# Kernel tuning notes

Hardware: AMD Instinct MI355X
Metric: run time of the kernel (lower is better)

The kernel has to match this reference:

```python
import jax, jax.numpy as jnp
import numpy as np

S, B, H = 2048, 2, 1024
NH = 16
HD = H // NH
EPS = 1e-5


def _ln(z, w, b):
    m = jnp.mean(z, axis=-1, keepdims=True)
    v = jnp.mean(jnp.square(z - m), axis=-1, keepdims=True)
    return (z - m) * jax.lax.rsqrt(v + EPS) * w + b


def setup_inputs() -> dict:
    key = jax.random.key(0)
    ks = jax.random.split(key, 8)
    std = 0.02
    return {
        "x": jax.random.normal(ks[0], (S, B, H), dtype=jnp.float32),
        "ln1_w": jnp.ones((H,), jnp.float32),
        "ln1_b": jnp.zeros((H,), jnp.float32),
        "w_qkv": jax.random.normal(ks[1], (3 * H, H), jnp.float32) * std,
        "b_qkv": jnp.zeros((3 * H,), jnp.float32),
        "w_proj": jax.random.normal(ks[2], (H, H), jnp.float32) * std,
        "b_proj": jnp.zeros((H,), jnp.float32),
        "ln2_w": jnp.ones((H,), jnp.float32),
        "ln2_b": jnp.zeros((H,), jnp.float32),
        "w_fc1": jax.random.normal(ks[3], (4 * H, H), jnp.float32) * std,
        "b_fc1": jnp.zeros((4 * H,), jnp.float32),
        "w_fc2": jax.random.normal(ks[4], (H, 4 * H), jnp.float32) * std,
        "b_fc2": jnp.zeros((H,), jnp.float32),
    }


def reference(x, ln1_w, ln1_b, w_qkv, b_qkv, w_proj, b_proj,
              ln2_w, ln2_b, w_fc1, b_fc1, w_fc2, b_fc2):
    s, b, h = x.shape
    # --- LayerNormLinear: LN then fused QKV projection ---
    residual = x
    qkv = _ln(x, ln1_w, ln1_b) @ w_qkv.T + b_qkv            # [S, B, 3H]
    # per-head interleaved packing: [S, B, NH, 3*HD] then split on last dim
    qkv = qkv.reshape(s, b, NH, 3 * HD).transpose(1, 2, 0, 3)  # [B, NH, S, 3HD]
    q, k, v = jnp.split(qkv, 3, axis=3)                      # each [B, NH, S, HD]
    # --- naive causal attention with full SxS scores ---
    scores = jnp.einsum("bhsd,bhtd->bhst", q, k) * (HD ** -0.5)
    causal = jnp.triu(jnp.ones((s, s), dtype=bool), k=1)
    scores = jnp.where(causal, -jnp.inf, scores)
    attn = jax.nn.softmax(scores, axis=-1)                   # [B, NH, S, S]
    out = jnp.einsum("bhst,bhtd->bhsd", attn, v)             # [B, NH, S, HD]
    out = out.transpose(0, 2, 1, 3).reshape(b, s, h).transpose(1, 0, 2)  # [S, B, H]
    out = out @ w_proj.T + b_proj
    x = residual + out
    # --- LayerNormMLP: LN -> fc1 -> gelu(tanh) -> fc2, residual ---
    residual = x
    hmid = jax.nn.gelu(_ln(x, ln2_w, ln2_b) @ w_fc1.T + b_fc1, approximate=True)
    x = residual + (hmid @ w_fc2.T + b_fc2)
    return x
```

## Files before the change

### kernel.cpp

```cpp
#include <hip/hip_runtime.h>
#include <math.h>

#define S_LEN 2048
#define B_SZ 2
#define NHEAD 16
#define HDIM 64
#define H_DIM 1024
#define M_ROWS (S_LEN * B_SZ)
#define LN_EPS 1e-5f
#define KSTR 72
#define SCL 0.18033688011112042f

typedef __attribute__((ext_vector_type(4))) float f32x4;
typedef __attribute__((ext_vector_type(8))) short short8;
typedef __attribute__((ext_vector_type(8))) unsigned short u16x8;
typedef __attribute__((ext_vector_type(4))) unsigned short u16x4;
typedef __attribute__((ext_vector_type(2))) unsigned short u16x2;

typedef __attribute__((address_space(3))) unsigned int lds_u32;
typedef const __attribute__((address_space(1))) unsigned int glb_u32;

__device__ __forceinline__ float bf2f(unsigned short u) {
    return __uint_as_float(((unsigned int)u) << 16);
}
__device__ __forceinline__ unsigned short f2bf(float f) {
    unsigned int u = __float_as_uint(f);
    return (unsigned short)((u + 0x7fffu + ((u >> 16) & 1u)) >> 16);
}

__global__ __launch_bounds__(256) void cast_all(const float* __restrict__ wqkv,
                                                const float* __restrict__ wproj,
                                                const float* __restrict__ wfc1,
                                                const float* __restrict__ wfc2,
                                                unsigned short* __restrict__ oqkv,
                                                unsigned short* __restrict__ oproj,
                                                unsigned short* __restrict__ ofc1,
                                                unsigned short* __restrict__ ofc2) {
    const int i = blockIdx.x * 256 + threadIdx.x;
    const float* src; unsigned short* dst; int off;
    if (i < 786432)       { src = wqkv;  dst = oqkv;  off = i; }
    else if (i < 1048576) { src = wproj; dst = oproj; off = i - 786432; }
    else if (i < 2097152) { src = wfc1;  dst = ofc1;  off = i - 1048576; }
    else                  { src = wfc2;  dst = ofc2;  off = i - 2097152; }
    f32x4 v = ((const f32x4*)src)[off];
    u16x4 o;
    o.x = f2bf(v.x); o.y = f2bf(v.y); o.z = f2bf(v.z); o.w = f2bf(v.w);
    ((u16x4*)dst)[off] = o;
}

__global__ __launch_bounds__(256) void ln_bf16(const float* __restrict__ x,
                                               const float* __restrict__ w,
                                               const float* __restrict__ b,
                                               unsigned short* __restrict__ y) {
    const int m = blockIdx.x;
    const int tid = threadIdx.x;
    const float* row = x + (size_t)m * H_DIM;

    float4 v = ((const float4*)row)[tid];
    float s  = v.x + v.y + v.z + v.w;
    float ss = v.x * v.x + v.y * v.y + v.z * v.z + v.w * v.w;

    __shared__ float rs[4], rss[4], stats[2];
    const int wave = tid >> 6, lane = tid & 63;
    for (int off = 32; off; off >>= 1) {
        s  += __shfl_down(s, off);
        ss += __shfl_down(ss, off);
    }
    if (lane == 0) { rs[wave] = s; rss[wave] = ss; }
    __syncthreads();
    if (tid == 0) {
        float S = rs[0] + rs[1] + rs[2] + rs[3];
        float SS = rss[0] + rss[1] + rss[2] + rss[3];
        float mean = S * (1.0f / H_DIM);
        float var = SS * (1.0f / H_DIM) - mean * mean;
        stats[0] = mean;
        stats[1] = rsqrtf(var + LN_EPS);
    }
    __syncthreads();
    const float mean = stats[0], inv = stats[1];
    float4 wv = ((const float4*)w)[tid];
    float4 bv = ((const float4*)b)[tid];
    u16x4 o;
    o.x = f2bf((v.x - mean) * inv * wv.x + bv.x);
    o.y = f2bf((v.y - mean) * inv * wv.y + bv.y);
    o.z = f2bf((v.z - mean) * inv * wv.z + bv.z);
    o.w = f2bf((v.w - mean) * inv * wv.w + bv.w);
    ((u16x4*)(y + (size_t)m * H_DIM))[tid] = o;
}

template <int EPI, bool BF_OUT, int TN>
__global__ __launch_bounds__(256) void gemm_mfma(const unsigned short* __restrict__ A,
                                                 const unsigned short* __restrict__ B,
                                                 const float* __restrict__ bias,
                                                 const float* __restrict__ resid,
                                                 void* __restrict__ Cout,
                                                 int M, int N, int K) {
    constexpr int NJ  = TN / 32;
    constexpr int ANI = 4;
    constexpr int BNI = TN / 32;
    __shared__ __attribute__((aligned(16))) unsigned short As0[128 * 64];
    __shared__ __attribute__((aligned(16))) unsigned short Bs0[TN * 64];
    __shared__ __attribute__((aligned(16))) unsigned short As1[128 * 64];
    __shared__ __attribute__((aligned(16))) unsigned short Bs1[TN * 64];

    const int tid = threadIdx.x;
    const int wid = tid >> 6;
    const int ln  = tid & 63;
    const int quad = ln >> 4;
    const int mr   = ln & 15;
    const int wm = (wid >> 1) * 64;
    const int wn = (wid & 1) * (TN / 2);

    const int mb = M >> 7;
    const int stripe = mb >> 3;
    const int xcd = blockIdx.x & 7;
    const int local = blockIdx.x >> 3;
    const int m0 = (xcd * stripe + (local % stripe)) << 7;
    const int n0 = (local / stripe) * TN;

    const int lr = ln >> 3, lc = ln & 7;
    const size_t Kb = (size_t)K * 2;
    const char* gA = (const char*)A + (size_t)(m0 + wid * 32 + lr) * Kb
                     + (size_t)((lc << 4) ^ (lr << 4));
    const int bwr = (TN == 128) ? wid * 32 : wid * 16;
    const char* gB = (const char*)B + (size_t)(n0 + bwr + lr) * Kb
                     + (size_t)((lc << 4) ^ (lr << 4));

    auto stage = [&](int kt, unsigned short* As_, unsigned short* Bs_) {
        const char* pa = gA + (size_t)kt * 128;
        unsigned int* la = (unsigned int*)As_ + wid * (ANI * 256);
#pragma unroll
        for (int i = 0; i < ANI; i++)
            __builtin_amdgcn_global_load_lds((glb_u32*)(pa + (size_t)i * 8 * Kb),
                                             (lds_u32*)(la + i * 256), 16, 0, 0);
        const char* pb = gB + (size_t)kt * 128;
        unsigned int* lb = (unsigned int*)Bs_ + wid * (BNI * 256);
#pragma unroll
        for (int i = 0; i < BNI; i++)
            __builtin_amdgcn_global_load_lds((glb_u32*)(pb + (size_t)i * 8 * Kb),
                                             (lds_u32*)(lb + i * 256), 16, 0, 0);
    };

    const f32x4 zero = {0.f, 0.f, 0.f, 0.f};
    f32x4 acc[4][NJ];
#pragma unroll
    for (int i = 0; i < 4; i++)
#pragma unroll
        for (int j = 0; j < NJ; j++) acc[i][j] = zero;

    const int swz = (mr & 7) << 3;
    auto compute = [&](const unsigned short* As_, const unsigned short* Bs_) {
#pragma unroll
        for (int h = 0; h < 2; h++) {
            short8 af[4], bfr[NJ];
#pragma unroll
            for (int i = 0; i < 4; i++)
                af[i] = *(const short8*)(As_ + (wm + i * 16 + mr) * 64
                                             + ((h * 32 + quad * 8) ^ swz));
#pragma unroll
            for (int j = 0; j < NJ; j++)
                bfr[j] = *(const short8*)(Bs_ + (wn + j * 16 + mr) * 64
                                              + ((h * 32 + quad * 8) ^ swz));
#pragma unroll
            for (int i = 0; i < 4; i++)
#pragma unroll
                for (int j = 0; j < NJ; j++)
                    acc[i][j] = __builtin_amdgcn_mfma_f32_16x16x32_bf16(bfr[j], af[i], acc[i][j], 0, 0, 0);
        }
    };

    const int nt = K >> 6;
    stage(0, As0, Bs0);
    __syncthreads();
    for (int kt = 0; kt < nt; kt += 2) {
        stage(kt + 1, As1, Bs1);
        compute(As0, Bs0);
        __syncthreads();
        if (kt + 2 < nt) stage(kt + 2, As0, Bs0);
        compute(As1, Bs1);
        if (kt + 2 < nt) __syncthreads();
    }

    f32x4 bias4[NJ];
#pragma unroll
    for (int j = 0; j < NJ; j++)
        bias4[j] = *(const f32x4*)(bias + n0 + wn + j * 16 + quad * 4);

#pragma unroll
    for (int i = 0; i < 4; i++) {
        const int m = m0 + wm + i * 16 + mr;
#pragma unroll
        for (int j = 0; j < NJ; j++) {
            const int nb = n0 + wn + j * 16 + quad * 4;
            f32x4 v = acc[i][j] + bias4[j];
            if (EPI == 1) v += *(const f32x4*)(resid + (size_t)m * N + nb);
            if (EPI == 2) {
#pragma unroll
                for (int r = 0; r < 4; r++) {
                    const float t = v[r];
                    const float u = t + 0.044715f * t * t * t;
                    const float e = exp2f(2.3022112f * u);
                    v[r] = t - t / (e + 1.0f);
                }
            }
            if (BF_OUT) {
                u16x4 pk;
                pk.x = f2bf(v.x); pk.y = f2bf(v.y); pk.z = f2bf(v.z); pk.w = f2bf(v.w);
                *(u16x4*)((unsigned short*)Cout + (size_t)m * N + nb) = pk;
            } else {
                *(f32x4*)((float*)Cout + (size_t)m * N + nb) = v;
            }
        }
    }
}

__global__ __launch_bounds__(256) void attn_mfma(const unsigned short* __restrict__ qkv,
                                                 unsigned short* __restrict__ out) {
    __shared__ __attribute__((aligned(16))) unsigned short Ks[64 * KSTR];
    __shared__ __attribute__((aligned(16))) unsigned short Vs[64 * KSTR];
    __shared__ __attribute__((aligned(16))) unsigned short Ps[64 * KSTR];

    const int tid = threadIdx.x;
    const int wid = tid >> 6;
    const int ln  = tid & 63;
    const int quad = ln >> 4;
    const int mr   = ln & 15;

    const int id = blockIdx.x;
    const int local = id >> 3;
    const int bh = (id & 7) * 4 + (local >> 4);
    const int pa = local & 15;
    const int b  = bh >> 4;
    const int nh = bh & 15;
    const size_t chan = (size_t)nh * 192;

    const int ksr = tid >> 2, ksc = tid & 3;
    const int vt0 = (tid & 31) * 2, vd0 = (tid >> 5) * 8;

    u16x8 kp0, kp1, vp0, vp1;

#pragma unroll
    for (int half = 0; half < 2; half++) {
        const int qt = half ? (31 - pa) : pa;
        const int qb = qt * 64;

        short8 qf0, qf1;
        {
            const int qrow = qb + wid * 16 + mr;
            const unsigned short* gq = qkv + ((size_t)(qrow * 2 + b)) * 3072 + chan + quad * 8;
            qf0 = *(const short8*)gq;
            qf1 = *(const short8*)(gq + 32);
        }

        const f32x4 zero = {0.f, 0.f, 0.f, 0.f};
        f32x4 o[4];
        float ps = 0.f;
#pragma unroll
        for (int d = 0; d < 4; d++) o[d] = zero;

        {
            const unsigned short* gk = qkv + ((size_t)(ksr * 2 + b)) * 3072 + chan + 64 + ksc * 16;
            kp0 = *(const u16x8*)gk;
            kp1 = *(const u16x8*)(gk + 8);
            const unsigned short* gv = qkv + ((size_t)(vt0 * 2 + b)) * 3072 + chan + 128 + vd0;
            vp0 = *(const u16x8*)gv;
            vp1 = *(const u16x8*)(gv + 6144);
        }

        for (int kt = 0; kt <= qt; kt++) {
            __syncthreads();
            *(u16x8*)(Ks + ksr * KSTR + ksc * 16) = kp0;
            *(u16x8*)(Ks + ksr * KSTR + ksc * 16 + 8) = kp1;
#pragma unroll
            for (int j = 0; j < 8; j++) {
                u16x2 pr; pr.x = vp0[j]; pr.y = vp1[j];
                *(u16x2*)(Vs + (vd0 + j) * KSTR + vt0) = pr;
            }
            if (kt < qt) {
                const int nb = (kt + 1) * 64;
                const unsigned short* gk =
                    qkv + ((size_t)((nb + ksr) * 2 + b)) * 3072 + chan + 64 + ksc * 16;
                kp0 = *(const u16x8*)gk;
                kp1 = *(const u16x8*)(gk + 8);
                const unsigned short* gv =
                    qkv + ((size_t)((nb + vt0) * 2 + b)) * 3072 + chan + 128 + vd0;
                vp0 = *(const u16x8*)gv;
                vp1 = *(const u16x8*)(gv + 6144);
            }
            __syncthreads();

            f32x4 sacc[4];
#pragma unroll
            for (int n = 0; n < 4; n++) {
                sacc[n] = zero;
                const unsigned short* kb = Ks + (n * 16 + mr) * KSTR + quad * 8;
                short8 kfr0 = *(const short8*)kb;
                short8 kfr1 = *(const short8*)(kb + 32);
                sacc[n] = __builtin_amdgcn_mfma_f32_16x16x32_bf16(kfr0, qf0, sacc[n], 0, 0, 0);
                sacc[n] = __builtin_amdgcn_mfma_f32_16x16x32_bf16(kfr1, qf1, sacc[n], 0, 0, 0);
            }
            if (kt == qt) {
#pragma unroll
                for (int n = 0; n < 4; n++)
#pragma unroll
                    for (int r = 0; r < 4; r++)
                        if (n * 16 + quad * 4 + r > wid * 16 + mr) sacc[n][r] = -3.0e38f;
            }

            unsigned short* prow = Ps + (wid * 16 + mr) * KSTR + quad * 4;
#pragma unroll
            for (int n = 0; n < 4; n++) {
                u16x4 pk;
#pragma unroll
                for (int r = 0; r < 4; r++) {
                    const float p = exp2f(fminf(sacc[n][r] * SCL, 80.f));
                    ps += p;
                    pk[r] = (unsigned short)(__float_as_uint(p) >> 16);
                }
                *(u16x4*)(prow + n * 16) = pk;
            }

            {
                const unsigned short* pb = Ps + (wid * 16 + mr) * KSTR + quad * 8;
                short8 pa0 = *(const short8*)pb;
                short8 pa1 = *(const short8*)(pb + 32);
#pragma unroll
                for (int d = 0; d < 4; d++) {
                    const unsigned short* vb = Vs + (d * 16 + mr) * KSTR + quad * 8;
                    short8 vf0 = *(const short8*)vb;
                    short8 vf1 = *(const short8*)(vb + 32);
                    o[d] = __builtin_amdgcn_mfma_f32_16x16x32_bf16(vf0, pa0, o[d], 0, 0, 0);
                    o[d] = __builtin_amdgcn_mfma_f32_16x16x32_bf16(vf1, pa1, o[d], 0, 0, 0);
                }
            }
        }

        ps += __shfl_xor(ps, 16);
        ps += __shfl_xor(ps, 32);
        const float inv = 1.0f / ps;
        const int qrow = qb + wid * 16 + mr;
        unsigned short* po = out + ((size_t)(qrow * 2 + b)) * H_DIM + nh * HDIM;
#pragma unroll
        for (int d = 0; d < 4; d++) {
            u16x4 pk;
#pragma unroll
            for (int r = 0; r < 4; r++) pk[r] = f2bf(o[d][r] * inv);
            *(u16x4*)(po + d * 16 + quad * 4) = pk;
        }
    }
}

extern "C" void kernel_launch(void* const* d_in, const int* in_sizes, int n_in,
                              void* d_out, int out_size, void* d_ws, size_t ws_size,
                              hipStream_t stream) {
    const float* x      = (const float*)d_in[0];
    const float* ln1_w  = (const float*)d_in[1];
    const float* ln1_b  = (const float*)d_in[2];
    const float* w_qkv  = (const float*)d_in[3];
    const float* b_qkv  = (const float*)d_in[4];
    const float* w_proj = (const float*)d_in[5];
    const float* b_proj = (const float*)d_in[6];
    const float* ln2_w  = (const float*)d_in[7];
    const float* ln2_b  = (const float*)d_in[8];
    const float* w_fc1  = (const float*)d_in[9];
    const float* b_fc1  = (const float*)d_in[10];
    const float* w_fc2  = (const float*)d_in[11];
    const float* b_fc2  = (const float*)d_in[12];
    float* out = (float*)d_out;

    char* ws = (char*)d_ws;
    unsigned short* wqkv_bf  = (unsigned short*)(ws);
    unsigned short* wproj_bf = (unsigned short*)(ws + ((size_t)6 << 20));
    unsigned short* wfc1_bf  = (unsigned short*)(ws + ((size_t)8 << 20));
    unsigned short* wfc2_bf  = (unsigned short*)(ws + ((size_t)16 << 20));
    unsigned short* ln_buf   = (unsigned short*)(ws + ((size_t)24 << 20));
    unsigned short* qkv_bf   = (unsigned short*)(ws + ((size_t)32 << 20));
    unsigned short* attn_bf  = (unsigned short*)(ws + ((size_t)56 << 20));
    unsigned short* fc1_bf   = (unsigned short*)(ws + ((size_t)32 << 20));

    cast_all<<<12288, 256, 0, stream>>>(w_qkv, w_proj, w_fc1, w_fc2,
                                        wqkv_bf, wproj_bf, wfc1_bf, wfc2_bf);

    ln_bf16<<<M_ROWS, 256, 0, stream>>>(x, ln1_w, ln1_b, ln_buf);
    gemm_mfma<0, true, 128><<<768, 256, 0, stream>>>(
        ln_buf, wqkv_bf, b_qkv, nullptr, qkv_bf, M_ROWS, 3072, 1024);
    attn_mfma<<<512, 256, 0, stream>>>(qkv_bf, attn_bf);
    gemm_mfma<1, false, 64><<<512, 256, 0, stream>>>(
        attn_bf, wproj_bf, b_proj, x, out, M_ROWS, 1024, 1024);
    ln_bf16<<<M_ROWS, 256, 0, stream>>>(out, ln2_w, ln2_b, ln_buf);
    gemm_mfma<2, true, 128><<<1024, 256, 0, stream>>>(
        ln_buf, wfc1_bf, b_fc1, nullptr, fc1_bf, M_ROWS, 4096, 1024);
    gemm_mfma<1, false, 64><<<512, 256, 0, stream>>>(
        fc1_bf, wfc2_bf, b_fc2, out, out, M_ROWS, 1024, 4096);
}
```

Before: 344.5 us.

## Use multi-buffered GEMM pipeline with explicit vmcnt waits

Restructures the MFMA GEMM main loop from a double-buffer, two-barrier scheme into a ring of 2 or 3 LDS buffers (3 when TN is 64). Each iteration waits with an explicit s_waitcnt vmcnt count so only the current tile's async global-to-LDS loads must be complete, and later tiles stay in flight. The goal is to hide more global load latency behind compute. In exchange it uses more LDS per block, which can lower occupancy, and its correctness depends on hand-computed vmcnt constants matching the number of issued loads.

```diff
diff --git a/kernel.cpp b/kernel.cpp
--- a/kernel.cpp
+++ b/kernel.cpp
@@ -19,6 +19,8 @@
 
 typedef __attribute__((address_space(3))) unsigned int lds_u32;
 typedef const __attribute__((address_space(1))) unsigned int glb_u32;
+
+#define ASM_VMCNT(N) asm volatile("s_waitcnt vmcnt(" #N ")" ::: "memory")
 
 __device__ __forceinline__ float bf2f(unsigned short u) {
     return __uint_as_float(((unsigned int)u) << 16);
@@ -98,10 +100,9 @@
     constexpr int NJ  = TN / 32;
     constexpr int ANI = 4;
     constexpr int BNI = TN / 32;
-    __shared__ __attribute__((aligned(16))) unsigned short As0[128 * 64];
-    __shared__ __attribute__((aligned(16))) unsigned short Bs0[TN * 64];
-    __shared__ __attribute__((aligned(16))) unsigned short As1[128 * 64];
-    __shared__ __attribute__((aligned(16))) unsigned short Bs1[TN * 64];
+    constexpr int NBUF = (TN == 128) ? 2 : 3;
+    __shared__ __attribute__((aligned(16))) unsigned short As[NBUF][128 * 64];
+    __shared__ __attribute__((aligned(16))) unsigned short Bs[NBUF][TN * 64];
 
     const int tid = threadIdx.x;
     const int wid = tid >> 6;
@@ -126,15 +127,15 @@
     const char* gB = (const char*)B + (size_t)(n0 + bwr + lr) * Kb
                      + (size_t)((lc << 4) ^ (lr << 4));
 
-    auto stage = [&](int kt, unsigned short* As_, unsigned short* Bs_) {
+    auto stage = [&](int kt, int buf) {
         const char* pa = gA + (size_t)kt * 128;
-        unsigned int* la = (unsigned int*)As_ + wid * (ANI * 256);
+        unsigned int* la = (unsigned int*)&As[buf][0] + wid * (ANI * 256);
 #pragma unroll
         for (int i = 0; i < ANI; i++)
             __builtin_amdgcn_global_load_lds((glb_u32*)(pa + (size_t)i * 8 * Kb),
                                              (lds_u32*)(la + i * 256), 16, 0, 0);
         const char* pb = gB + (size_t)kt * 128;
-        unsigned int* lb = (unsigned int*)Bs_ + wid * (BNI * 256);
+        unsigned int* lb = (unsigned int*)&Bs[buf][0] + wid * (BNI * 256);
 #pragma unroll
         for (int i = 0; i < BNI; i++)
             __builtin_amdgcn_global_load_lds((glb_u32*)(pb + (size_t)i * 8 * Kb),
@@ -170,15 +171,27 @@
     };
 
     const int nt = K >> 6;
-    stage(0, As0, Bs0);
-    __syncthreads();
-    for (int kt = 0; kt < nt; kt += 2) {
-        stage(kt + 1, As1, Bs1);
-        compute(As0, Bs0);
-        __syncthreads();
-        if (kt + 2 < nt) stage(kt + 2, As0, Bs0);
-        compute(As1, Bs1);
-        if (kt + 2 < nt) __syncthreads();
+    stage(0, 0);
+    stage(1, 1);
+    if (NBUF == 3) stage(2, 2);
+
+    int cb = 0;
+    for (int kt = 0; kt < nt; kt++) {
+        if (NBUF == 3) {
+            if (kt + 2 < nt)      ASM_VMCNT(12);
+            else if (kt + 1 < nt) ASM_VMCNT(6);
+            else                  ASM_VMCNT(0);
+        } else {
+            if (kt + 1 < nt)      ASM_VMCNT(8);
+            else                  ASM_VMCNT(0);
+        }
+        __builtin_amdgcn_s_barrier();
+        __builtin_amdgcn_sched_barrier(0);
+        compute(&As[cb][0], &Bs[cb][0]);
+        __builtin_amdgcn_sched_barrier(0);
+        __builtin_amdgcn_s_barrier();
+        if (kt + NBUF < nt) stage(kt + NBUF, cb);
+        cb = (cb + 1 == NBUF) ? 0 : cb + 1;
     }
 
     f32x4 bias4[NJ];
```

Result: no change. 339.2 us (-1.5%).

## Load GEMM B operand directly into registers and hand-pipeline A staging with vmcnt waits

Applied to the files above, without the earlier changes.

The GEMM no longer stages B tiles through LDS. Each lane reads its B fragments straight from global memory into registers one k-tile ahead, while A stays double-buffered in LDS via global_load_lds. Explicit s_waitcnt vmcnt counts, raw s_barrier and sched_barrier replace __syncthreads so loads overlap compute, and launch bounds request 3 blocks per CU. This cuts LDS traffic and footprint, but the B global loads are less coalesced, register pressure rises, and the hand-tuned vmcnt counts are fragile to get right.

```diff
diff --git a/kernel.cpp b/kernel.cpp
--- a/kernel.cpp
+++ b/kernel.cpp
@@ -19,6 +19,8 @@
 
 typedef __attribute__((address_space(3))) unsigned int lds_u32;
 typedef const __attribute__((address_space(1))) unsigned int glb_u32;
+
+#define ASM_VMCNT(N) asm volatile("s_waitcnt vmcnt(" #N ")" ::: "memory")
 
 __device__ __forceinline__ float bf2f(unsigned short u) {
     return __uint_as_float(((unsigned int)u) << 16);
@@ -89,19 +91,15 @@
 }
 
 template <int EPI, bool BF_OUT, int TN>
-__global__ __launch_bounds__(256) void gemm_mfma(const unsigned short* __restrict__ A,
-                                                 const unsigned short* __restrict__ B,
-                                                 const float* __restrict__ bias,
-                                                 const float* __restrict__ resid,
-                                                 void* __restrict__ Cout,
-                                                 int M, int N, int K) {
+__global__ __launch_bounds__(256, 3) void gemm_mfma(const unsigned short* __restrict__ A,
+                                                    const unsigned short* __restrict__ B,
+                                                    const float* __restrict__ bias,
+                                                    const float* __restrict__ resid,
+                                                    void* __restrict__ Cout,
+                                                    int M, int N, int K) {
     constexpr int NJ  = TN / 32;
     constexpr int ANI = 4;
-    constexpr int BNI = TN / 32;
-    __shared__ __attribute__((aligned(16))) unsigned short As0[128 * 64];
-    __shared__ __attribute__((aligned(16))) unsigned short Bs0[TN * 64];
-    __shared__ __attribute__((aligned(16))) unsigned short As1[128 * 64];
-    __shared__ __attribute__((aligned(16))) unsigned short Bs1[TN * 64];
+    __shared__ __attribute__((aligned(16))) unsigned short As[2][128 * 64];
 
     const int tid = threadIdx.x;
     const int wid = tid >> 6;
@@ -122,23 +120,24 @@
     const size_t Kb = (size_t)K * 2;
     const char* gA = (const char*)A + (size_t)(m0 + wid * 32 + lr) * Kb
                      + (size_t)((lc << 4) ^ (lr << 4));
-    const int bwr = (TN == 128) ? wid * 32 : wid * 16;
-    const char* gB = (const char*)B + (size_t)(n0 + bwr + lr) * Kb
-                     + (size_t)((lc << 4) ^ (lr << 4));
-
-    auto stage = [&](int kt, unsigned short* As_, unsigned short* Bs_) {
+
+    auto stageA = [&](int kt, int buf) {
         const char* pa = gA + (size_t)kt * 128;
-        unsigned int* la = (unsigned int*)As_ + wid * (ANI * 256);
+        unsigned int* la = (unsigned int*)&As[buf][0] + wid * (ANI * 256);
 #pragma unroll
         for (int i = 0; i < ANI; i++)
             __builtin_amdgcn_global_load_lds((glb_u32*)(pa + (size_t)i * 8 * Kb),
                                              (lds_u32*)(la + i * 256), 16, 0, 0);
-        const char* pb = gB + (size_t)kt * 128;
-        unsigned int* lb = (unsigned int*)Bs_ + wid * (BNI * 256);
-#pragma unroll
-        for (int i = 0; i < BNI; i++)
-            __builtin_amdgcn_global_load_lds((glb_u32*)(pb + (size_t)i * 8 * Kb),
-                                             (lds_u32*)(lb + i * 256), 16, 0, 0);
+    };
+
+    const unsigned short* gBl = B + (size_t)(n0 + wn + mr) * K + quad * 8;
+    u16x8 b0[NJ][2], b1[NJ][2];
+    auto loadB = [&](int kt, u16x8 (&bb)[NJ][2]) {
+#pragma unroll
+        for (int j = 0; j < NJ; j++)
+#pragma unroll
+            for (int h = 0; h < 2; h++)
+                bb[j][h] = *(const u16x8*)(gBl + (size_t)(j * 16) * K + kt * 64 + h * 32);
     };
 
     const f32x4 zero = {0.f, 0.f, 0.f, 0.f};
@@ -149,36 +148,47 @@
         for (int j = 0; j < NJ; j++) acc[i][j] = zero;
 
     const int swz = (mr & 7) << 3;
-    auto compute = [&](const unsigned short* As_, const unsigned short* Bs_) {
+    auto compute = [&](const unsigned short* As_, u16x8 (&bb)[NJ][2]) {
 #pragma unroll
         for (int h = 0; h < 2; h++) {
-            short8 af[4], bfr[NJ];
+            short8 af[4];
 #pragma unroll
             for (int i = 0; i < 4; i++)
                 af[i] = *(const short8*)(As_ + (wm + i * 16 + mr) * 64
                                              + ((h * 32 + quad * 8) ^ swz));
 #pragma unroll
-            for (int j = 0; j < NJ; j++)
-                bfr[j] = *(const short8*)(Bs_ + (wn + j * 16 + mr) * 64
-                                              + ((h * 32 + quad * 8) ^ swz));
-#pragma unroll
             for (int i = 0; i < 4; i++)
 #pragma unroll
                 for (int j = 0; j < NJ; j++)
-                    acc[i][j] = __builtin_amdgcn_mfma_f32_16x16x32_bf16(bfr[j], af[i], acc[i][j], 0, 0, 0);
+                    acc[i][j] = __builtin_amdgcn_mfma_f32_16x16x32_bf16(
+                        (short8)bb[j][h], af[i], acc[i][j], 0, 0, 0);
         }
     };
 
     const int nt = K >> 6;
-    stage(0, As0, Bs0);
-    __syncthreads();
+    stageA(0, 0);
+    loadB(0, b0);
+    stageA(1, 1);
+
     for (int kt = 0; kt < nt; kt += 2) {
-        stage(kt + 1, As1, Bs1);
-        compute(As0, Bs0);
-        __syncthreads();
-        if (kt + 2 < nt) stage(kt + 2, As0, Bs0);
-        compute(As1, Bs1);
-        if (kt + 2 < nt) __syncthreads();
+        if (TN == 128) { if (kt + 2 < nt) ASM_VMCNT(12); else ASM_VMCNT(8); }
+        else           { if (kt + 2 < nt) ASM_VMCNT(8);  else ASM_VMCNT(4); }
+        __builtin_amdgcn_s_barrier();
+        if (kt + 1 < nt) loadB(kt + 1, b1);
+        __builtin_amdgcn_sched_barrier(0);
+        compute(&As[0][0], b0);
+        __builtin_amdgcn_sched_barrier(0);
+        __builtin_amdgcn_s_barrier();
+        if (kt + 2 < nt) stageA(kt + 2, 0);
+        if (TN == 128) { if (kt + 3 < nt) ASM_VMCNT(12); else ASM_VMCNT(8); }
+        else           { if (kt + 3 < nt) ASM_VMCNT(8);  else ASM_VMCNT(4); }
+        __builtin_amdgcn_s_barrier();
+        if (kt + 2 < nt) loadB(kt + 2, b0);
+        __builtin_amdgcn_sched_barrier(0);
+        compute(&As[1][0], b1);
+        __builtin_amdgcn_sched_barrier(0);
+        __builtin_amdgcn_s_barrier();
+        if (kt + 3 < nt) stageA(kt + 3, 1);
     }
 
     f32x4 bias4[NJ];
```

Result: slower. 511.1 us (+48.4%).
